# Kernel tuning notes

Measured on AMD Instinct MI355X. Metric: run time of the kernel, lower is better.

Reference implementation:

```python
import jax, jax.numpy as jnp
import numpy as np
from jax import lax

WBITS = 2
ABITS = 2
STRIDES = (1, 1)
PADDING = 'SAME'


def _ste_quantize(x, k):
    # round(x * n) / n with straight-through gradient (identity)
    n = float(2 ** k - 1)
    q = jnp.round(x * n) / n
    return x + lax.stop_gradient(q - x)


def _quantize_weight(w, k):
    # DoReFa-style weight quantization: tanh, normalize to [0,1], quantize, map to [-1,1]
    t = jnp.tanh(w)
    t = t / jnp.max(jnp.abs(t)) * 0.5 + 0.5
    return 2.0 * _ste_quantize(t, k) - 1.0


def _quantize_act(x, k):
    return _ste_quantize(jnp.clip(x, 0.0, 1.0), k)


def setup_inputs() -> dict:
    key = jax.random.key(0)
    kx, kw = jax.random.split(key)
    x = jax.random.uniform(kx, (32, 56, 56, 256), dtype=jnp.float32)  # NHWC
    w = jax.random.normal(kw, (3, 3, 256, 256), dtype=jnp.float32) * 0.2  # HWIO
    # match init normalization: unit L2 norm per output channel over (h,w,cin)
    w = w / jnp.sqrt(1e-7 + jnp.sum(w * w, axis=(0, 1, 2), keepdims=True))
    return {'x': x, 'w': w}


def reference(x, w) -> jnp.ndarray:
    wq = _quantize_weight(w, WBITS)        # low-bit weights in [-1, 1]
    xq = _quantize_act(x, ABITS)           # low-bit activations in [0, 1]
    out = lax.conv_general_dilated(
        xq, wq,
        window_strides=STRIDES,
        padding=PADDING,
        dimension_numbers=('NHWC', 'HWIO', 'NHWC'),
    )
    return out
```

## Files before the change

kernel.cpp:

```cpp
#include <hip/hip_runtime.h>
#include <stdint.h>

#define GLOBAL_AS __attribute__((address_space(1)))
#define LDS_AS    __attribute__((address_space(3)))

typedef int v4i  __attribute__((ext_vector_type(4)));
typedef int v16i __attribute__((ext_vector_type(16)));

__device__ __forceinline__ void gload_lds16(const void* g, void* l) {
    __builtin_amdgcn_global_load_lds((GLOBAL_AS uint32_t*)g, (LDS_AS uint32_t*)l, 16, 0, 0);
}

__global__ void k_wmax(const float* __restrict__ w, unsigned* __restrict__ maxbits, int n) {
    int i = blockIdx.x * blockDim.x + threadIdx.x;
    int stride = gridDim.x * blockDim.x;
    float m = 0.f;
    for (; i < n; i += stride) m = fmaxf(m, fabsf(tanhf(w[i])));
#pragma unroll
    for (int off = 32; off > 0; off >>= 1)
        m = fmaxf(m, __shfl_xor(m, off, 64));
    if ((threadIdx.x & 63) == 0) atomicMax(maxbits, __float_as_uint(m));
}

__global__ void k_wq(const float* __restrict__ w, const unsigned* __restrict__ maxbits,
                     int8_t* __restrict__ wqt) {
    int t = blockIdx.x * 256 + threadIdx.x;
    int co = t & 255;
    int kblk = t >> 8;
    float inv = 0.5f / __uint_as_float(*maxbits);
    int8_t b[16];
#pragma unroll
    for (int i = 0; i < 16; ++i) {
        float tv = tanhf(w[(long)(kblk * 16 + i) * 256 + co]);
        int qi = (int)rintf((tv * inv + 0.5f) * 3.0f);
        b[i] = (int8_t)(2 * qi - 3);
    }
    *(int4*)(wqt + (long)co * 2304 + kblk * 16) = *(int4*)b;
}

__global__ void k_xq(const float* __restrict__ x, int8_t* __restrict__ xqp) {
    int t = blockIdx.x * 256 + threadIdx.x;
    int g  = t & 15;
    int p  = t >> 4;
    int xp = p % 58;
    int q  = p / 58;
    int yp = q % 58;
    int n  = q / 58;
    int4 r;
    if (yp == 0 || yp == 57 || xp == 0 || xp == 57) {
        r = make_int4(0, 0, 0, 0);
    } else {
        const float4* px = (const float4*)(x + (((long)((n * 56 + (yp - 1)) * 56 + (xp - 1))) << 8) + g * 16);
        int wds[4];
#pragma unroll
        for (int jj = 0; jj < 4; ++jj) {
            float4 v = px[jj];
            int b0 = (int)rintf(fminf(fmaxf(v.x, 0.f), 1.f) * 3.f);
            int b1 = (int)rintf(fminf(fmaxf(v.y, 0.f), 1.f) * 3.f);
            int b2 = (int)rintf(fminf(fmaxf(v.z, 0.f), 1.f) * 3.f);
            int b3 = (int)rintf(fminf(fmaxf(v.w, 0.f), 1.f) * 3.f);
            wds[jj] = b0 | (b1 << 8) | (b2 << 16) | (b3 << 24);
        }
        r = make_int4(wds[0], wds[1], wds[2], wds[3]);
    }
    *(int4*)(xqp + ((long)t << 4)) = r;
}

#define BM 128
#define BN 128

__global__ __launch_bounds__(256) void k_conv(const int8_t* __restrict__ xqp,
                                              const int8_t* __restrict__ wqt,
                                              float* __restrict__ out) {
    __shared__ int8_t sA[BM * 128];
    __shared__ int8_t sB[BN * 128];

    const int tid    = threadIdx.x;
    const int wv     = tid >> 6;
    const int lane   = tid & 63;
    const int mBase  = blockIdx.x * BM;
    const int coBase = blockIdx.y * BN;

    const int lr = lane >> 3;
    const int lp = lane & 7;
    const int8_t* aB[4];
    const int8_t* bB[4];
#pragma unroll
    for (int j = 0; j < 4; ++j) {
        int r = wv * 8 + j * 32 + lr;
        int g = lp ^ (r & 7);
        int m = mBase + r;
        int n = m / 3136;
        int rem = m - n * 3136;
        int y = rem / 56;
        int x = rem - y * 56;
        aB[j] = xqp + (((long)((n * 58 + y) * 58 + x)) << 8) + g * 16;
        bB[j] = wqt + (long)(coBase + r) * 2304 + g * 16;
    }

    v16i acc[2][2];
#pragma unroll
    for (int a = 0; a < 2; ++a)
#pragma unroll
        for (int b = 0; b < 2; ++b)
#pragma unroll
            for (int r = 0; r < 16; ++r) acc[a][b][r] = 0;

    const int wm  = (wv & 1) * 64;
    const int wn  = (wv >> 1) * 64;
    const int l31 = lane & 31;
    const int hi  = lane >> 5;

    const int rA0 = wm + l31,      rA1 = wm + 32 + l31;
    const int rB0 = wn + l31,      rB1 = wn + 32 + l31;
    const int8_t* aF0 = sA + rA0 * 128;  const int axr0 = (rA0 & 7) << 4;
    const int8_t* aF1 = sA + rA1 * 128;  const int axr1 = (rA1 & 7) << 4;
    const int8_t* bF0 = sB + rB0 * 128;  const int bxr0 = (rB0 & 7) << 4;
    const int8_t* bF1 = sB + rB1 * 128;  const int bxr1 = (rB1 & 7) << 4;

    for (int iter = 0; iter < 18; ++iter) {
        const int tap  = iter >> 1;
        const int ky   = tap / 3;
        const int kx   = tap - ky * 3;
        const int half = (iter & 1) * 128;
        const int aOff = (((ky * 58) + kx) << 8) + half;
        const int bOff = tap * 256 + half;

        __syncthreads();
#pragma unroll
        for (int j = 0; j < 4; ++j) {
            gload_lds16(aB[j] + aOff, sA + (wv * 8 + j * 32) * 128);
            gload_lds16(bB[j] + bOff, sB + (wv * 8 + j * 32) * 128);
        }
        __syncthreads();

#pragma unroll
        for (int kk = 0; kk < 4; ++kk) {
            const int kc = (kk * 2 + hi) << 4;
            v4i a0 = *(const v4i*)(aF0 + (kc ^ axr0));
            v4i a1 = *(const v4i*)(aF1 + (kc ^ axr1));
            v4i b0 = *(const v4i*)(bF0 + (kc ^ bxr0));
            v4i b1 = *(const v4i*)(bF1 + (kc ^ bxr1));
            acc[0][0] = __builtin_amdgcn_mfma_i32_32x32x32_i8(a0, b0, acc[0][0], 0, 0, 0);
            acc[0][1] = __builtin_amdgcn_mfma_i32_32x32x32_i8(a0, b1, acc[0][1], 0, 0, 0);
            acc[1][0] = __builtin_amdgcn_mfma_i32_32x32x32_i8(a1, b0, acc[1][0], 0, 0, 0);
            acc[1][1] = __builtin_amdgcn_mfma_i32_32x32x32_i8(a1, b1, acc[1][1], 0, 0, 0);
        }
    }

    const float s = 1.0f / 9.0f;
#pragma unroll
    for (int mt = 0; mt < 2; ++mt) {
#pragma unroll
        for (int nt = 0; nt < 2; ++nt) {
            const int ocol = coBase + wn + nt * 32 + l31;
#pragma unroll
            for (int reg = 0; reg < 16; ++reg) {
                const int row = (reg & 3) + 8 * (reg >> 2) + 4 * hi;
                const long orow = mBase + wm + mt * 32 + row;
                out[orow * 256 + ocol] = (float)acc[mt][nt][reg] * s;
            }
        }
    }
}

extern "C" void kernel_launch(void* const* d_in, const int* in_sizes, int n_in,
                              void* d_out, int out_size, void* d_ws, size_t ws_size,
                              hipStream_t stream) {
    const float* x = (const float*)d_in[0];
    const float* w = (const float*)d_in[1];
    float* out = (float*)d_out;

    unsigned* maxbits = (unsigned*)d_ws;
    int8_t* wqt = (int8_t*)d_ws + 4096;
    int8_t* xqp = (int8_t*)d_ws + 4096 + 589824;

    hipMemsetAsync(maxbits, 0, 4, stream);
    k_wmax<<<256, 256, 0, stream>>>(w, maxbits, 3 * 3 * 256 * 256);
    k_wq<<<144, 256, 0, stream>>>(w, maxbits, wqt);
    k_xq<<<6728, 256, 0, stream>>>(x, xqp);
    dim3 grid(784, 2);
    k_conv<<<grid, 256, 0, stream>>>(xqp, wqt, out);
}
```

Before: 275.7 us.

## Double-buffer LDS tiles in int8 conv to overlap global loads with MFMA

Shared memory for the A and B tiles is doubled. Each iteration now issues the direct global-to-LDS loads for the next K slice before computing on the current one, and a partial vmcnt wait lets the previous loads complete while the new ones stay in flight. This hides global load latency behind the MFMA work. In exchange, LDS use per block rises to 64KB, which may reduce occupancy, and correctness depends on the hand-written waitcnt and barrier placement.

```diff
diff --git a/kernel.cpp b/kernel.cpp
--- a/kernel.cpp
+++ b/kernel.cpp
@@ -72,8 +72,8 @@
 __global__ __launch_bounds__(256) void k_conv(const int8_t* __restrict__ xqp,
                                               const int8_t* __restrict__ wqt,
                                               float* __restrict__ out) {
-    __shared__ int8_t sA[BM * 128];
-    __shared__ int8_t sB[BN * 128];
+    __shared__ int8_t sA[2][BM * 128];
+    __shared__ int8_t sB[2][BN * 128];
 
     const int tid    = threadIdx.x;
     const int wv     = tid >> 6;
@@ -111,42 +111,57 @@
     const int l31 = lane & 31;
     const int hi  = lane >> 5;
 
-    const int rA0 = wm + l31,      rA1 = wm + 32 + l31;
-    const int rB0 = wn + l31,      rB1 = wn + 32 + l31;
-    const int8_t* aF0 = sA + rA0 * 128;  const int axr0 = (rA0 & 7) << 4;
-    const int8_t* aF1 = sA + rA1 * 128;  const int axr1 = (rA1 & 7) << 4;
-    const int8_t* bF0 = sB + rB0 * 128;  const int bxr0 = (rB0 & 7) << 4;
-    const int8_t* bF1 = sB + rB1 * 128;  const int bxr1 = (rB1 & 7) << 4;
+    const int rA0 = (wm + l31) * 128;       const int axr0 = ((wm + l31) & 7) << 4;
+    const int rA1 = (wm + 32 + l31) * 128;  const int axr1 = ((wm + 32 + l31) & 7) << 4;
+    const int rB0 = (wn + l31) * 128;       const int bxr0 = ((wn + l31) & 7) << 4;
+    const int rB1 = (wn + 32 + l31) * 128;  const int bxr1 = ((wn + 32 + l31) & 7) << 4;
 
-    for (int iter = 0; iter < 18; ++iter) {
-        const int tap  = iter >> 1;
-        const int ky   = tap / 3;
-        const int kx   = tap - ky * 3;
-        const int half = (iter & 1) * 128;
-        const int aOff = (((ky * 58) + kx) << 8) + half;
-        const int bOff = tap * 256 + half;
-
-        __syncthreads();
+    auto issue = [&](int it, int b) {
+        int tap = it >> 1;
+        int ky  = tap / 3;
+        int kx  = tap - ky * 3;
+        int aOff = ((ky * 58 + kx) << 8) + (it & 1) * 128;
+        int bOff = tap * 256 + (it & 1) * 128;
 #pragma unroll
         for (int j = 0; j < 4; ++j) {
-            gload_lds16(aB[j] + aOff, sA + (wv * 8 + j * 32) * 128);
-            gload_lds16(bB[j] + bOff, sB + (wv * 8 + j * 32) * 128);
+            gload_lds16(aB[j] + aOff, &sA[b][(wv * 8 + j * 32) * 128]);
+            gload_lds16(bB[j] + bOff, &sB[b][(wv * 8 + j * 32) * 128]);
         }
-        __syncthreads();
+    };
 
+    auto compute = [&](int b) {
+        const int8_t* pA = sA[b];
+        const int8_t* pB = sB[b];
 #pragma unroll
         for (int kk = 0; kk < 4; ++kk) {
             const int kc = (kk * 2 + hi) << 4;
-            v4i a0 = *(const v4i*)(aF0 + (kc ^ axr0));
-            v4i a1 = *(const v4i*)(aF1 + (kc ^ axr1));
-            v4i b0 = *(const v4i*)(bF0 + (kc ^ bxr0));
-            v4i b1 = *(const v4i*)(bF1 + (kc ^ bxr1));
+            v4i a0 = *(const v4i*)(pA + rA0 + (kc ^ axr0));
+            v4i a1 = *(const v4i*)(pA + rA1 + (kc ^ axr1));
+            v4i b0 = *(const v4i*)(pB + rB0 + (kc ^ bxr0));
+            v4i b1 = *(const v4i*)(pB + rB1 + (kc ^ bxr1));
             acc[0][0] = __builtin_amdgcn_mfma_i32_32x32x32_i8(a0, b0, acc[0][0], 0, 0, 0);
             acc[0][1] = __builtin_amdgcn_mfma_i32_32x32x32_i8(a0, b1, acc[0][1], 0, 0, 0);
             acc[1][0] = __builtin_amdgcn_mfma_i32_32x32x32_i8(a1, b0, acc[1][0], 0, 0, 0);
             acc[1][1] = __builtin_amdgcn_mfma_i32_32x32x32_i8(a1, b1, acc[1][1], 0, 0, 0);
         }
+    };
+
+    issue(0, 0);
+#pragma unroll 2
+    for (int it = 0; it < 17; ++it) {
+        issue(it + 1, (it + 1) & 1);
+        asm volatile("s_waitcnt vmcnt(8)" ::: "memory");
+        __builtin_amdgcn_s_barrier();
+        asm volatile("" ::: "memory");
+        compute(it & 1);
+        asm volatile("" ::: "memory");
+        __builtin_amdgcn_s_barrier();
+        asm volatile("" ::: "memory");
     }
+    asm volatile("s_waitcnt vmcnt(0)" ::: "memory");
+    __builtin_amdgcn_s_barrier();
+    asm volatile("" ::: "memory");
+    compute(1);
 
     const float s = 1.0f / 9.0f;
 #pragma unroll
```

Measured after the change: 267.5 us. -3.0%, faster.

## Load MFMA operands directly from global memory, dropping LDS staging

Applied to the files above, without the earlier changes.

The conv kernel no longer stages A/B tiles in shared memory with direct-to-LDS loads and block barriers. Each lane now reads its MFMA fragments straight from global memory, relying on L1/L2 for reuse. All 9 taps are unrolled, and launch bounds request 3 blocks per CU. This removes the barrier stalls and LDS traffic, but multiplies global/L1 load requests since each fragment is re-fetched by every wave that uses it.

```diff
diff --git a/kernel.cpp b/kernel.cpp
--- a/kernel.cpp
+++ b/kernel.cpp
@@ -1,15 +1,8 @@
 #include <hip/hip_runtime.h>
 #include <stdint.h>
 
-#define GLOBAL_AS __attribute__((address_space(1)))
-#define LDS_AS    __attribute__((address_space(3)))
-
 typedef int v4i  __attribute__((ext_vector_type(4)));
 typedef int v16i __attribute__((ext_vector_type(16)));
-
-__device__ __forceinline__ void gload_lds16(const void* g, void* l) {
-    __builtin_amdgcn_global_load_lds((GLOBAL_AS uint32_t*)g, (LDS_AS uint32_t*)l, 16, 0, 0);
-}
 
 __global__ void k_wmax(const float* __restrict__ w, unsigned* __restrict__ maxbits, int n) {
     int i = blockIdx.x * blockDim.x + threadIdx.x;
@@ -69,33 +62,31 @@
 #define BM 128
 #define BN 128
 
-__global__ __launch_bounds__(256) void k_conv(const int8_t* __restrict__ xqp,
-                                              const int8_t* __restrict__ wqt,
-                                              float* __restrict__ out) {
-    __shared__ int8_t sA[BM * 128];
-    __shared__ int8_t sB[BN * 128];
-
+__global__ __launch_bounds__(256, 3) void k_conv(const int8_t* __restrict__ xqp,
+                                                 const int8_t* __restrict__ wqt,
+                                                 float* __restrict__ out) {
     const int tid    = threadIdx.x;
     const int wv     = tid >> 6;
     const int lane   = tid & 63;
     const int mBase  = blockIdx.x * BM;
     const int coBase = blockIdx.y * BN;
+    const int wm  = (wv & 1) * 64;
+    const int wn  = (wv >> 1) * 64;
+    const int l31 = lane & 31;
+    const int hi  = lane >> 5;
 
-    const int lr = lane >> 3;
-    const int lp = lane & 7;
-    const int8_t* aB[4];
-    const int8_t* bB[4];
+    const int8_t* aR[2];
+    const int8_t* bC[2];
 #pragma unroll
-    for (int j = 0; j < 4; ++j) {
-        int r = wv * 8 + j * 32 + lr;
-        int g = lp ^ (r & 7);
-        int m = mBase + r;
+    for (int t = 0; t < 2; ++t) {
+        int m = mBase + wm + t * 32 + l31;
         int n = m / 3136;
         int rem = m - n * 3136;
         int y = rem / 56;
         int x = rem - y * 56;
-        aB[j] = xqp + (((long)((n * 58 + y) * 58 + x)) << 8) + g * 16;
-        bB[j] = wqt + (long)(coBase + r) * 2304 + g * 16;
+        aR[t] = xqp + (((long)((n * 58 + y) * 58 + x)) << 8) + hi * 16;
+        int c = coBase + wn + t * 32 + l31;
+        bC[t] = wqt + (long)c * 2304 + hi * 16;
     }
 
     v16i acc[2][2];
@@ -106,45 +97,24 @@
 #pragma unroll
             for (int r = 0; r < 16; ++r) acc[a][b][r] = 0;
 
-    const int wm  = (wv & 1) * 64;
-    const int wn  = (wv >> 1) * 64;
-    const int l31 = lane & 31;
-    const int hi  = lane >> 5;
-
-    const int rA0 = wm + l31,      rA1 = wm + 32 + l31;
-    const int rB0 = wn + l31,      rB1 = wn + 32 + l31;
-    const int8_t* aF0 = sA + rA0 * 128;  const int axr0 = (rA0 & 7) << 4;
-    const int8_t* aF1 = sA + rA1 * 128;  const int axr1 = (rA1 & 7) << 4;
-    const int8_t* bF0 = sB + rB0 * 128;  const int bxr0 = (rB0 & 7) << 4;
-    const int8_t* bF1 = sB + rB1 * 128;  const int bxr1 = (rB1 & 7) << 4;
-
-    for (int iter = 0; iter < 18; ++iter) {
-        const int tap  = iter >> 1;
-        const int ky   = tap / 3;
-        const int kx   = tap - ky * 3;
-        const int half = (iter & 1) * 128;
-        const int aOff = (((ky * 58) + kx) << 8) + half;
-        const int bOff = tap * 256 + half;
-
-        __syncthreads();
 #pragma unroll
-        for (int j = 0; j < 4; ++j) {
-            gload_lds16(aB[j] + aOff, sA + (wv * 8 + j * 32) * 128);
-            gload_lds16(bB[j] + bOff, sB + (wv * 8 + j * 32) * 128);
-        }
-        __syncthreads();
-
+    for (int ky = 0; ky < 3; ++ky) {
 #pragma unroll
-        for (int kk = 0; kk < 4; ++kk) {
-            const int kc = (kk * 2 + hi) << 4;
-            v4i a0 = *(const v4i*)(aF0 + (kc ^ axr0));
-            v4i a1 = *(const v4i*)(aF1 + (kc ^ axr1));
-            v4i b0 = *(const v4i*)(bF0 + (kc ^ bxr0));
-            v4i b1 = *(const v4i*)(bF1 + (kc ^ bxr1));
-            acc[0][0] = __builtin_amdgcn_mfma_i32_32x32x32_i8(a0, b0, acc[0][0], 0, 0, 0);
-            acc[0][1] = __builtin_amdgcn_mfma_i32_32x32x32_i8(a0, b1, acc[0][1], 0, 0, 0);
-            acc[1][0] = __builtin_amdgcn_mfma_i32_32x32x32_i8(a1, b0, acc[1][0], 0, 0, 0);
-            acc[1][1] = __builtin_amdgcn_mfma_i32_32x32x32_i8(a1, b1, acc[1][1], 0, 0, 0);
+        for (int kx = 0; kx < 3; ++kx) {
+            const int aOff = (ky * 58 + kx) << 8;
+            const int bOff = (ky * 3 + kx) << 8;
+#pragma unroll
+            for (int kk = 0; kk < 8; ++kk) {
+                const int ko = kk * 32;
+                v4i a0 = *(const v4i*)(aR[0] + aOff + ko);
+                v4i a1 = *(const v4i*)(aR[1] + aOff + ko);
+                v4i b0 = *(const v4i*)(bC[0] + bOff + ko);
+                v4i b1 = *(const v4i*)(bC[1] + bOff + ko);
+                acc[0][0] = __builtin_amdgcn_mfma_i32_32x32x32_i8(a0, b0, acc[0][0], 0, 0, 0);
+                acc[0][1] = __builtin_amdgcn_mfma_i32_32x32x32_i8(a0, b1, acc[0][1], 0, 0, 0);
+                acc[1][0] = __builtin_amdgcn_mfma_i32_32x32x32_i8(a1, b0, acc[1][0], 0, 0, 0);
+                acc[1][1] = __builtin_amdgcn_mfma_i32_32x32x32_i8(a1, b1, acc[1][1], 0, 0, 0);
+            }
         }
     }
 
```

Result: slower. 421.8 us (+53.0%).
